# Kernel tuning notes

Measured on AMD Instinct MI355X. Metric: run time of the kernel, lower is better.

Reference implementation:

```python
import jax, jax.numpy as jnp
import numpy as np

NUM_CLASSES = 2
TOP_K = 1500
CONF_THRESH = 0.01
NMS_THRESH = 0.2
VAR0, VAR1 = 0.1, 0.2  # cfg['variance']


def setup_inputs() -> dict:
    key = jax.random.key(0)
    k1, k2, k3 = jax.random.split(key, 3)
    B, P = 32, 76800
    loc_data = jax.random.normal(k1, (B, P, 4), jnp.float32)
    conf_data = jax.random.uniform(k2, (B * P, NUM_CLASSES), jnp.float32)
    prior_data = jax.random.uniform(k3, (P, 4), jnp.float32)
    return {"loc_data": loc_data, "conf_data": conf_data, "prior_data": prior_data}


def _decode(loc, priors):
    # loc, priors: [P,4]; SSD box decode with variances
    cxcy = priors[:, :2] + loc[:, :2] * VAR0 * priors[:, 2:]
    wh = priors[:, 2:] * jnp.exp(loc[:, 2:] * VAR1)
    x1y1 = cxcy - wh * 0.5
    return jnp.concatenate([x1y1, x1y1 + wh], axis=-1)  # [P,4] (x1,y1,x2,y2)


def _nms_per_class(scores, boxes):
    # scores: [P], boxes: [P,4] -> [TOP_K,5] packed (score,x1,y1,x2,y2)
    s = jnp.where(scores > CONF_THRESH, scores, -jnp.inf)
    sk, idx = jax.lax.top_k(s, TOP_K)  # torch nms keeps only top_k candidates
    bk = boxes[idx]
    x1, y1, x2, y2 = bk[:, 0], bk[:, 1], bk[:, 2], bk[:, 3]
    area = (x2 - x1) * (y2 - y1)
    iota = jnp.arange(TOP_K)

    def step(active, i):
        # greedy NMS over score-descending candidates
        xx1 = jnp.maximum(x1, x1[i]); yy1 = jnp.maximum(y1, y1[i])
        xx2 = jnp.minimum(x2, x2[i]); yy2 = jnp.minimum(y2, y2[i])
        inter = jnp.maximum(xx2 - xx1, 0.0) * jnp.maximum(yy2 - yy1, 0.0)
        iou = inter / (area + area[i] - inter)
        kept = active[i]
        suppress = (iou > NMS_THRESH) & (iota != i)
        active = jnp.where(kept, active & ~suppress, active)
        return active, kept

    _, keep = jax.lax.scan(step, sk > -jnp.inf, iota)
    rows = jnp.where(keep[:, None], jnp.concatenate([sk[:, None], bk], axis=1), 0.0)
    # pack kept rows at the front (score-descending order), zeros after
    rank = jnp.cumsum(keep) - 1
    dest = jnp.where(keep, rank, TOP_K)  # dump non-kept into scratch slot
    return jnp.zeros((TOP_K + 1, 5), bk.dtype).at[dest].set(rows)[:TOP_K]


def reference(loc_data, conf_data, prior_data):
    B, P, _ = loc_data.shape
    conf = conf_data.reshape(B, P, NUM_CLASSES)
    decoded = jax.vmap(_decode, in_axes=(0, None))(loc_data, prior_data)  # [B,P,4]
    outs = []
    for cl in range(1, NUM_CLASSES):  # background class 0 stays zero
        outs.append(jax.vmap(_nms_per_class)(conf[:, :, cl], decoded))
    bg = jnp.zeros((B, 1, TOP_K, 5), decoded.dtype)
    return jnp.concatenate([bg, jnp.stack(outs, axis=1)], axis=1)  # [B,C,TOP_K,5]
```

## Files before the change

### kernel.cpp

```cpp
#include <hip/hip_runtime.h>
#include <stdint.h>

typedef unsigned long long u64;
typedef unsigned int u32;

#define NUM_B 32
#define NUM_P 76800
#define TOPK 1500
#define NBINS 4096
#define CAP 2048
#define NWORDS 24
#define NCHUNK 6
#define CPAD 32
#define HSLICES 16
#define HCHUNK (NUM_P / HSLICES)

__device__ __forceinline__ u32 fbits(float f) { return __float_as_uint(f); }
__device__ __forceinline__ int binOf(float s) {
    int b = (int)(s * (float)NBINS);
    return (b > NBINS - 1) ? NBINS - 1 : b;
}
__device__ __forceinline__ u64 readlane64(u64 v, int l) {
    u32 lo = (u32)__builtin_amdgcn_readlane((int)(u32)(v & 0xffffffffu), l);
    u32 hi = (u32)__builtin_amdgcn_readlane((int)(u32)(v >> 32), l);
    return ((u64)hi << 32) | lo;
}

__global__ __launch_bounds__(256) void hist_kernel(const float4* __restrict__ conf4,
                                                   u32* __restrict__ hist,
                                                   u32* __restrict__ counts) {
    int c = blockIdx.x, b = blockIdx.y, tid = threadIdx.x;
    if (c == 0 && tid < CPAD) counts[(size_t)b * CPAD + tid] = 0;
    __shared__ u32 h[NBINS];
    for (int i = tid; i < NBINS; i += 256) h[i] = 0;
    __syncthreads();
    const float4* base = conf4 + (size_t)b * (NUM_P / 2) + (size_t)c * (HCHUNK / 2);
    for (int i = tid; i < HCHUNK / 2; i += 256) {
        float4 v = base[i];
        if (v.y > 0.01f) atomicAdd(&h[binOf(v.y)], 1u);
        if (v.w > 0.01f) atomicAdd(&h[binOf(v.w)], 1u);
    }
    __syncthreads();
    u32* outp = hist + ((size_t)b * HSLICES + c) * NBINS;
    for (int i = tid; i < NBINS; i += 256) outp[i] = h[i];
}

__global__ void thresh_kernel(const u32* __restrict__ hist, int* __restrict__ tbin) {
    int b = blockIdx.x;
    int tid = threadIdx.x;
    const u32* hb = hist + (size_t)b * HSLICES * NBINS;
    __shared__ u32 vals[256];
    __shared__ int s_min;
    u32 total = 0;
    for (int c = 0; c < NBINS / 256; ++c) {
        if (tid == 0) s_min = 256;
        int bin = NBINS - 1 - (c * 256 + tid);
        u32 v = 0;
#pragma unroll
        for (int s = 0; s < HSLICES; ++s) v += hb[(size_t)s * NBINS + bin];
        __syncthreads();
        vals[tid] = v;
        __syncthreads();
        for (int off = 1; off < 256; off <<= 1) {
            u32 add = (tid >= off) ? vals[tid - off] : 0;
            __syncthreads();
            vals[tid] += add;
            __syncthreads();
        }
        u32 cum = total + vals[tid];
        if (cum >= TOPK) atomicMin(&s_min, tid);
        __syncthreads();
        if (s_min < 256) {
            if (tid == 0) tbin[b] = NBINS - 1 - (c * 256 + s_min);
            return;
        }
        total += vals[255];
    }
    if (tid == 0) tbin[b] = 0;
}

__global__ __launch_bounds__(256) void compact_kernel(
    const float4* __restrict__ conf4, const int* __restrict__ tbin,
    u32* __restrict__ counts, u64* __restrict__ keys) {
    int b = blockIdx.y;
    int tid = threadIdx.x;
    int lane = tid & 63, wave = tid >> 6;
    int f4 = blockIdx.x * 256 + tid;
    float4 c = conf4[(size_t)b * (NUM_P / 2) + f4];
    int tb = tbin[b];
    int p0 = f4 * 2, p1 = p0 + 1;
    bool v0 = (c.y > 0.01f) && (binOf(c.y) >= tb);
    bool v1 = (c.w > 0.01f) && (binOf(c.w) >= tb);

    u64 m0 = __ballot(v0), m1 = __ballot(v1);
    u32 c0 = (u32)__popcll(m0);
    u64 below = (1ULL << lane) - 1ULL;
    u32 off0 = (u32)__popcll(m0 & below);
    u32 off1 = c0 + (u32)__popcll(m1 & below);
    u32 wtot = c0 + (u32)__popcll(m1);

    __shared__ u32 wcnt[4];
    __shared__ u32 s_base;
    if (lane == 0) wcnt[wave] = wtot;
    __syncthreads();
    if (tid == 0) {
        u32 tot = wcnt[0] + wcnt[1] + wcnt[2] + wcnt[3];
        s_base = (tot > 0) ? atomicAdd(&counts[(size_t)b * CPAD], tot) : 0u;
    }
    __syncthreads();
    u32 woff = 0;
    for (int w = 0; w < wave; ++w) woff += wcnt[w];
    if (v0) {
        u32 pos = s_base + woff + off0;
        if (pos < CAP) keys[(size_t)b * CAP + pos] = ((u64)fbits(c.y) << 32) | (u32)(~p0);
    }
    if (v1) {
        u32 pos = s_base + woff + off1;
        if (pos < CAP) keys[(size_t)b * CAP + pos] = ((u64)fbits(c.w) << 32) | (u32)(~p1);
    }
}

__global__ __launch_bounds__(256) void rank_decode_kernel(
    const u64* __restrict__ keys, const u32* __restrict__ counts,
    const float* __restrict__ loc, const float* __restrict__ prior,
    float* __restrict__ sscore, float* __restrict__ sbox) {
#pragma clang fp contract(off)
    int blk = blockIdx.x, b = blockIdx.y, tid = threadIdx.x;
    __shared__ u64 k[CAP];
    int n = (int)min(counts[(size_t)b * CPAD], (u32)CAP);
    for (int t = tid; t < CAP; t += 256)
        k[t] = (t < n) ? keys[(size_t)b * CAP + t] : 0ULL;
    __syncthreads();

    int t = blk * 256 + tid;
    u64 mykey = k[t];
    if (mykey == 0ULL) return;

    u32 rank = 0;
#pragma unroll 8
    for (int j = 0; j < CAP; ++j) rank += (k[j] > mykey) ? 1u : 0u;

    if (rank < TOPK) {
        u32 pidx = ~(u32)mykey;
        float sc = __uint_as_float((u32)(mykey >> 32));
        const float* lp = &loc[((size_t)b * NUM_P + pidx) * 4];
        const float* pp = &prior[(size_t)pidx * 4];
        float lx = lp[0], ly = lp[1], lw = lp[2], lh = lp[3];
        float pcx = pp[0], pcy = pp[1], pw = pp[2], ph = pp[3];
        float cx = pcx + (lx * 0.1f) * pw;
        float cy = pcy + (ly * 0.1f) * ph;
        float w  = pw * expf(lw * 0.2f);
        float h  = ph * expf(lh * 0.2f);
        float x1 = cx - w * 0.5f;
        float y1 = cy - h * 0.5f;
        float x2 = x1 + w;
        float y2 = y1 + h;
        sscore[(size_t)b * TOPK + rank] = sc;
        float* bx = &sbox[((size_t)b * TOPK + rank) * 4];
        bx[0] = x1; bx[1] = y1; bx[2] = x2; bx[3] = y2;
    }
}

__global__ __launch_bounds__(256) void mask_kernel(
    const float* __restrict__ sbox, u64* __restrict__ mask) {
#pragma clang fp contract(off)
    int w = blockIdx.x, c = blockIdx.y, b = blockIdx.z, tid = threadIdx.x;
    int i = c * 256 + tid;
    if ((w * 64 + 63) <= (c * 256)) return;
    __shared__ float4 cbox[64];
    __shared__ float car[64];
    if (tid < 64) {
        int j = w * 64 + tid;
        float4 bx = make_float4(0.f, 0.f, 0.f, 0.f);
        if (j < TOPK) bx = ((const float4*)sbox)[(size_t)b * TOPK + j];
        cbox[tid] = bx;
        car[tid] = (bx.z - bx.x) * (bx.w - bx.y);
    }
    __syncthreads();
    if (i < TOPK && (w * 64 + 63) > i) {
        const double MID = 0.5 * ((double)__uint_as_float(0x3E4CCCCDu) +
                                  (double)__uint_as_float(0x3E4CCCCEu));
        const float4 bx = ((const float4*)sbox)[(size_t)b * TOPK + i];
        float x1i = bx.x, y1i = bx.y, x2i = bx.z, y2i = bx.w;
        float ai = (x2i - x1i) * (y2i - y1i);
        u64 jmask = (i < w * 64) ? ~0ULL : (~0ULL << (i - w * 64 + 1));
        u64 m = 0;
        for (int j2 = 0; j2 < 64; ++j2) {
            float4 cb = cbox[j2];
            float xx1 = fmaxf(cb.x, x1i);
            float yy1 = fmaxf(cb.y, y1i);
            float xx2 = fminf(cb.z, x2i);
            float yy2 = fminf(cb.w, y2i);
            float iw = fmaxf(xx2 - xx1, 0.0f);
            float ih = fmaxf(yy2 - yy1, 0.0f);
            float inter = iw * ih;
            float denom = (car[j2] + ai) - inter;
            if ((double)inter >= MID * (double)denom) m |= (1ULL << j2);
        }
        m &= jmask;
        mask[((size_t)b * NWORDS + w) * TOPK + i] = m;
    }
}

__global__ __launch_bounds__(256) void sweep_kernel(
    const u64* __restrict__ mask, const float* __restrict__ sscore,
    const float* __restrict__ sbox, float* __restrict__ out) {
    int b = blockIdx.x, tid = threadIdx.x;
    int lane = tid & 63, wid = tid >> 6;

    const u64* mbase = mask + (size_t)b * NWORDS * TOPK;

    __shared__ u64 rowbuf[3][NWORDS][65];
    __shared__ u64 aw[NWORDS];
    __shared__ u32 pfx[NWORDS + 1];

    u64 act = 0;
    u64 sv[8];
    if (wid == 0) {
        for (int c = 0; c < NWORDS; ++c) {
            int r = c * 64 + lane;
            bool v = (r < TOPK) && (sscore[(size_t)b * TOPK + r] > 0.0f);
            u64 m = __ballot(v);
            if (lane == c) act = m;
        }
    } else {
        int w0 = (wid - 1) * 8;
#pragma unroll
        for (int t = 0; t < 2; ++t) {
            u64 tmp[8];
#pragma unroll
            for (int k = 0; k < 8; ++k)
                tmp[k] = (w0 + k >= t) ? mbase[(size_t)(w0 + k) * TOPK + t * 64 + lane] : 0ULL;
#pragma unroll
            for (int k = 0; k < 8; ++k)
                rowbuf[t][w0 + k][lane] = tmp[k];
        }
        {
            int rr = 2 * 64 + lane;
#pragma unroll
            for (int k = 0; k < 8; ++k)
                sv[k] = (w0 + k >= 2) ? mbase[(size_t)(w0 + k) * TOPK + rr] : 0ULL;
        }
    }
    __syncthreads();

    for (int T = 0; T < NWORDS; ++T) {
        if (wid == 0) {
            u64 dreg = rowbuf[T % 3][T][lane];
            u64 actw = readlane64(act, T);
            u64 kept = 0, rem = actw;
            while (rem) {
                int i2 = __ffsll(rem) - 1;
                kept |= (1ULL << i2);
                rem &= rem - 1;
                rem &= ~readlane64(dreg, i2);
            }
            if (lane == T) act = kept;
            if (lane > T && lane < NWORDS) {
                u64 kb = kept;
                while (kb) {
                    int r = __ffsll(kb) - 1;
                    kb &= kb - 1;
                    act &= ~rowbuf[T % 3][lane][r];
                }
            }
        } else {
            int tw = T + 2;
            if (tw < NWORDS) {
                int w0 = (wid - 1) * 8;
#pragma unroll
                for (int k = 0; k < 8; ++k)
                    rowbuf[tw % 3][w0 + k][lane] = sv[k];
                int tn = T + 3;
                if (tn < NWORDS) {
                    int rr = tn * 64 + lane;
                    bool vr = rr < TOPK;
#pragma unroll
                    for (int k = 0; k < 8; ++k)
                        sv[k] = (vr && (w0 + k >= tn))
                                    ? mbase[(size_t)(w0 + k) * TOPK + rr] : 0ULL;
                }
            }
        }
        __syncthreads();
    }

    if (wid == 0 && lane < NWORDS) aw[lane] = act;
    {
        float* p0 = out + ((size_t)b * 2 + 0) * TOPK * 5;
        float* p1 = out + ((size_t)b * 2 + 1) * TOPK * 5;
        for (int t = tid; t < TOPK * 5; t += 256) { p0[t] = 0.0f; p1[t] = 0.0f; }
    }
    __syncthreads();
    if (tid == 0) {
        u32 acc = 0;
        for (int wd = 0; wd < NWORDS; ++wd) { pfx[wd] = acc; acc += (u32)__popcll(aw[wd]); }
        pfx[NWORDS] = acc;
    }
    __syncthreads();
    for (int r = tid; r < TOPK; r += 256) {
        int wd = r >> 6;
        u64 word = aw[wd];
        if ((word >> (r & 63)) & 1ULL) {
            u32 rank = pfx[wd] + (u32)__popcll(word & ((1ULL << (r & 63)) - 1ULL));
            float sc = sscore[(size_t)b * TOPK + r];
            float4 bx = ((const float4*)sbox)[(size_t)b * TOPK + r];
            size_t base_o = (((size_t)b * 2 + 1) * TOPK + (size_t)rank) * 5;
            out[base_o + 0] = sc;
            out[base_o + 1] = bx.x;
            out[base_o + 2] = bx.y;
            out[base_o + 3] = bx.z;
            out[base_o + 4] = bx.w;
        }
    }
}

extern "C" void kernel_launch(void* const* d_in, const int* in_sizes, int n_in,
                              void* d_out, int out_size, void* d_ws, size_t ws_size,
                              hipStream_t stream) {
    const float* loc   = (const float*)d_in[0];
    const float* conf  = (const float*)d_in[1];
    const float* prior = (const float*)d_in[2];
    float* out = (float*)d_out;
    char* ws = (char*)d_ws;

    u64* mask_buf = (u64*)(ws + 0);
    u32* hist     = (u32*)(ws + 0);
    u64* keys     = (u64*)(ws + 8388608);
    u32* counts   = (u32*)(ws + 8912896);
    int* tbin     = (int*)(ws + 8916992);
    float* sscore = (float*)(ws + 9216000);
    float* sbox   = (float*)(ws + 9408000);

    hist_kernel<<<dim3(HSLICES, 32), 256, 0, stream>>>((const float4*)conf, hist, counts);
    thresh_kernel<<<32, 256, 0, stream>>>(hist, tbin);
    compact_kernel<<<dim3(150, 32), 256, 0, stream>>>((const float4*)conf, tbin, counts, keys);
    rank_decode_kernel<<<dim3(CAP / 256, 32), 256, 0, stream>>>(keys, counts, loc, prior,
                                                                sscore, sbox);
    mask_kernel<<<dim3(NWORDS, NCHUNK, 32), 256, 0, stream>>>(sbox, mask_buf);
    sweep_kernel<<<32, 256, 0, stream>>>(mask_buf, sscore, sbox, out);
}
```

Measured before the change: 194.3 us.

## Fuse mask and sweep kernels using a last-block-done atomic counter

```diff
diff --git a/kernel.cpp b/kernel.cpp
--- a/kernel.cpp
+++ b/kernel.cpp
@@ -11,6 +11,7 @@
 #define CAP 2048
 #define NWORDS 24
 #define NCHUNK 6
+#define MBLOCKS (NWORDS * NCHUNK)
 #define CPAD 32
 #define HSLICES 16
 #define HCHUNK (NUM_P / HSLICES)
@@ -28,9 +29,13 @@
 
 __global__ __launch_bounds__(256) void hist_kernel(const float4* __restrict__ conf4,
                                                    u32* __restrict__ hist,
-                                                   u32* __restrict__ counts) {
+                                                   u32* __restrict__ counts,
+                                                   u32* __restrict__ done) {
     int c = blockIdx.x, b = blockIdx.y, tid = threadIdx.x;
-    if (c == 0 && tid < CPAD) counts[(size_t)b * CPAD + tid] = 0;
+    if (c == 0 && tid < CPAD) {
+        counts[(size_t)b * CPAD + tid] = 0;
+        done[(size_t)b * CPAD + tid] = 0;
+    }
     __shared__ u32 h[NBINS];
     for (int i = tid; i < NBINS; i += 256) h[i] = 0;
     __syncthreads();
@@ -161,92 +166,93 @@
     }
 }
 
-__global__ __launch_bounds__(256) void mask_kernel(
-    const float* __restrict__ sbox, u64* __restrict__ mask) {
+__global__ __launch_bounds__(256) void mask_sweep_kernel(
+    const float* __restrict__ sbox, const float* __restrict__ sscore,
+    u64* __restrict__ mask, u32* __restrict__ done, float* __restrict__ out) {
 #pragma clang fp contract(off)
     int w = blockIdx.x, c = blockIdx.y, b = blockIdx.z, tid = threadIdx.x;
+    int lane = tid & 63, wid = tid >> 6;
     int i = c * 256 + tid;
-    if ((w * 64 + 63) <= (c * 256)) return;
+
     __shared__ float4 cbox[64];
     __shared__ float car[64];
-    if (tid < 64) {
-        int j = w * 64 + tid;
-        float4 bx = make_float4(0.f, 0.f, 0.f, 0.f);
-        if (j < TOPK) bx = ((const float4*)sbox)[(size_t)b * TOPK + j];
-        cbox[tid] = bx;
-        car[tid] = (bx.z - bx.x) * (bx.w - bx.y);
-    }
-    __syncthreads();
-    if (i < TOPK && (w * 64 + 63) > i) {
-        const double MID = 0.5 * ((double)__uint_as_float(0x3E4CCCCDu) +
-                                  (double)__uint_as_float(0x3E4CCCCEu));
-        const float4 bx = ((const float4*)sbox)[(size_t)b * TOPK + i];
-        float x1i = bx.x, y1i = bx.y, x2i = bx.z, y2i = bx.w;
-        float ai = (x2i - x1i) * (y2i - y1i);
-        u64 jmask = (i < w * 64) ? ~0ULL : (~0ULL << (i - w * 64 + 1));
-        u64 m = 0;
-        for (int j2 = 0; j2 < 64; ++j2) {
-            float4 cb = cbox[j2];
-            float xx1 = fmaxf(cb.x, x1i);
-            float yy1 = fmaxf(cb.y, y1i);
-            float xx2 = fminf(cb.z, x2i);
-            float yy2 = fminf(cb.w, y2i);
-            float iw = fmaxf(xx2 - xx1, 0.0f);
-            float ih = fmaxf(yy2 - yy1, 0.0f);
-            float inter = iw * ih;
-            float denom = (car[j2] + ai) - inter;
-            if ((double)inter >= MID * (double)denom) m |= (1ULL << j2);
-        }
-        m &= jmask;
-        mask[((size_t)b * NWORDS + w) * TOPK + i] = m;
-    }
-}
-
-__global__ __launch_bounds__(256) void sweep_kernel(
-    const u64* __restrict__ mask, const float* __restrict__ sscore,
-    const float* __restrict__ sbox, float* __restrict__ out) {
-    int b = blockIdx.x, tid = threadIdx.x;
-    int lane = tid & 63, wid = tid >> 6;
-
-    const u64* mbase = mask + (size_t)b * NWORDS * TOPK;
-
-    __shared__ u64 rowbuf[3][NWORDS][65];
+    __shared__ u64 rowbuf[2][NWORDS][65];
     __shared__ u64 aw[NWORDS];
     __shared__ u32 pfx[NWORDS + 1];
-
+    __shared__ u32 s_old;
+
+    bool blk_live = (w * 64 + 63) > (c * 256);
+    if (blk_live) {
+        if (tid < 64) {
+            int j = w * 64 + tid;
+            float4 bx = make_float4(0.f, 0.f, 0.f, 0.f);
+            if (j < TOPK) bx = ((const float4*)sbox)[(size_t)b * TOPK + j];
+            cbox[tid] = bx;
+            car[tid] = (bx.z - bx.x) * (bx.w - bx.y);
+        }
+        __syncthreads();
+        if (i < TOPK && (w * 64 + 63) > i) {
+            const double MID = 0.5 * ((double)__uint_as_float(0x3E4CCCCDu) +
+                                      (double)__uint_as_float(0x3E4CCCCEu));
+            const float4 bx = ((const float4*)sbox)[(size_t)b * TOPK + i];
+            float x1i = bx.x, y1i = bx.y, x2i = bx.z, y2i = bx.w;
+            float ai = (x2i - x1i) * (y2i - y1i);
+            u64 jmask = (i < w * 64) ? ~0ULL : (~0ULL << (i - w * 64 + 1));
+            u64 m = 0;
+            for (int j2 = 0; j2 < 64; ++j2) {
+                float4 cb = cbox[j2];
+                float xx1 = fmaxf(cb.x, x1i);
+                float yy1 = fmaxf(cb.y, y1i);
+                float xx2 = fminf(cb.z, x2i);
+                float yy2 = fminf(cb.w, y2i);
+                float iw = fmaxf(xx2 - xx1, 0.0f);
+                float ih = fmaxf(yy2 - yy1, 0.0f);
+                float inter = iw * ih;
+                float denom = (car[j2] + ai) - inter;
+                if ((double)inter >= MID * (double)denom) m |= (1ULL << j2);
+            }
+            m &= jmask;
+            mask[((size_t)b * NWORDS + w) * TOPK + i] = m;
+        }
+    }
+    __syncthreads();
+    if (tid == 0) {
+        __threadfence();
+        s_old = atomicAdd(&done[(size_t)b * CPAD], 1u);
+    }
+    __syncthreads();
+    if (s_old != MBLOCKS - 1) return;
+    __threadfence();
+
+    const u64* mbase = mask + (size_t)b * NWORDS * TOPK;
     u64 act = 0;
     u64 sv[8];
     if (wid == 0) {
-        for (int c = 0; c < NWORDS; ++c) {
-            int r = c * 64 + lane;
+        for (int cc = 0; cc < NWORDS; ++cc) {
+            int r = cc * 64 + lane;
             bool v = (r < TOPK) && (sscore[(size_t)b * TOPK + r] > 0.0f);
             u64 m = __ballot(v);
-            if (lane == c) act = m;
+            if (lane == cc) act = m;
         }
     } else {
         int w0 = (wid - 1) * 8;
-#pragma unroll
-        for (int t = 0; t < 2; ++t) {
-            u64 tmp[8];
-#pragma unroll
-            for (int k = 0; k < 8; ++k)
-                tmp[k] = (w0 + k >= t) ? mbase[(size_t)(w0 + k) * TOPK + t * 64 + lane] : 0ULL;
-#pragma unroll
-            for (int k = 0; k < 8; ++k)
-                rowbuf[t][w0 + k][lane] = tmp[k];
-        }
-        {
-            int rr = 2 * 64 + lane;
-#pragma unroll
-            for (int k = 0; k < 8; ++k)
-                sv[k] = (w0 + k >= 2) ? mbase[(size_t)(w0 + k) * TOPK + rr] : 0ULL;
-        }
+        u64 tmp[8];
+#pragma unroll
+        for (int k = 0; k < 8; ++k)
+            tmp[k] = mbase[(size_t)(w0 + k) * TOPK + lane];
+#pragma unroll
+        for (int k = 0; k < 8; ++k)
+            rowbuf[0][w0 + k][lane] = tmp[k];
+        int rr = 64 + lane;
+#pragma unroll
+        for (int k = 0; k < 8; ++k)
+            sv[k] = (w0 + k >= 1) ? mbase[(size_t)(w0 + k) * TOPK + rr] : 0ULL;
     }
     __syncthreads();
 
     for (int T = 0; T < NWORDS; ++T) {
         if (wid == 0) {
-            u64 dreg = rowbuf[T % 3][T][lane];
+            u64 dreg = rowbuf[T & 1][T][lane];
             u64 actw = readlane64(act, T);
             u64 kept = 0, rem = actw;
             while (rem) {
@@ -261,17 +267,17 @@
                 while (kb) {
                     int r = __ffsll(kb) - 1;
                     kb &= kb - 1;
-                    act &= ~rowbuf[T % 3][lane][r];
+                    act &= ~rowbuf[T & 1][lane][r];
                 }
             }
         } else {
-            int tw = T + 2;
+            int tw = T + 1;
             if (tw < NWORDS) {
                 int w0 = (wid - 1) * 8;
 #pragma unroll
                 for (int k = 0; k < 8; ++k)
-                    rowbuf[tw % 3][w0 + k][lane] = sv[k];
-                int tn = T + 3;
+                    rowbuf[tw & 1][w0 + k][lane] = sv[k];
+                int tn = T + 2;
                 if (tn < NWORDS) {
                     int rr = tn * 64 + lane;
                     bool vr = rr < TOPK;
@@ -331,12 +337,13 @@
     int* tbin     = (int*)(ws + 8916992);
     float* sscore = (float*)(ws + 9216000);
     float* sbox   = (float*)(ws + 9408000);
-
-    hist_kernel<<<dim3(HSLICES, 32), 256, 0, stream>>>((const float4*)conf, hist, counts);
+    u32* done     = (u32*)(ws + 10176000);
+
+    hist_kernel<<<dim3(HSLICES, 32), 256, 0, stream>>>((const float4*)conf, hist, counts, done);
     thresh_kernel<<<32, 256, 0, stream>>>(hist, tbin);
     compact_kernel<<<dim3(150, 32), 256, 0, stream>>>((const float4*)conf, tbin, counts, keys);
     rank_decode_kernel<<<dim3(CAP / 256, 32), 256, 0, stream>>>(keys, counts, loc, prior,
                                                                 sscore, sbox);
-    mask_kernel<<<dim3(NWORDS, NCHUNK, 32), 256, 0, stream>>>(sbox, mask_buf);
-    sweep_kernel<<<32, 256, 0, stream>>>(mask_buf, sscore, sbox, out);
-}
+    mask_sweep_kernel<<<dim3(NWORDS, NCHUNK, 32), 256, 0, stream>>>(sbox, sscore, mask_buf,
+                                                                    done, out);
+}
```

New measurement: 287.5 us. 1.48x slower.
